# Performance work log

Hardware: AMD Instinct MI355X
Metric: run time of the kernel (lower is better)

The kernel has to match this reference:

```python
import jax, jax.numpy as jnp
import numpy as np

B, N, D, YD = 256, 1024, 64, 2
EPS = 1e-7  # keras SCC epsilon clip


def interleave(x):
    # (B, L, ...): out[:,0::2]=first half, out[:,1::2]=second half
    b, L = x.shape[0], x.shape[1]
    a, c = x[:, : L // 2], x[:, L // 2:]
    return jnp.stack([a, c], axis=2).reshape((b, L) + x.shape[2:])


def block_interleave(x, scope):
    # tf.split into N//scope chunks of size `scope`, Interleave each, concat
    b, L = x.shape[0], x.shape[1]
    rest = x.shape[2:]
    xr = x.reshape((b, L // scope, 2, scope // 2) + rest)
    xr = jnp.swapaxes(xr, 2, 3)
    return xr.reshape((b, L) + rest)


def split_even_odd(x):
    # returns (odd, even) = (x[:,0::2], x[:,1::2])
    return x[:, 0::2], x[:, 1::2]


def mlp2(x, W1, b1, W2, b2):
    return jnp.dot(jax.nn.relu(jnp.dot(x, W1) + b1), W2) + b2


def emb2llr(e, W, b):
    return jax.nn.softmax(jnp.dot(e, W) + b, axis=-1)


def scce(v, p):
    # v: (B,L,1) int labels, p: (B,L,2) probs -> (B,L) per-element NLL
    pt = jnp.take_along_axis(p, v, axis=-1)[..., 0]
    return -jnp.log(jnp.clip(pt, EPS, 1.0))


def setup_inputs() -> dict:
    key = jax.random.key(0)
    ks = jax.random.split(key, 16)
    s = lambda fan: 1.0 / np.sqrt(fan)
    return {
        "x": jax.random.randint(ks[0], (B, N, 1), 0, 2, dtype=jnp.int32),
        "y": jax.random.normal(ks[1], (B, N, YD), dtype=jnp.float32),
        "emb_W": jax.random.normal(ks[2], (YD, D), dtype=jnp.float32) * s(YD),
        "emb_b": jnp.zeros((D,), jnp.float32),
        "lab_emb": jax.random.normal(ks[3], (2, D), dtype=jnp.float32) * s(D),
        "cn_W1": jax.random.normal(ks[4], (2 * D, D), dtype=jnp.float32) * s(2 * D),
        "cn_b1": jnp.zeros((D,), jnp.float32),
        "cn_W2": jax.random.normal(ks[5], (D, D), dtype=jnp.float32) * s(D),
        "cn_b2": jnp.zeros((D,), jnp.float32),
        "bn_W1": jax.random.normal(ks[6], (3 * D, D), dtype=jnp.float32) * s(3 * D),
        "bn_b1": jnp.zeros((D,), jnp.float32),
        "bn_W2": jax.random.normal(ks[7], (D, D), dtype=jnp.float32) * s(D),
        "bn_b2": jnp.zeros((D,), jnp.float32),
        "llr_W": jax.random.normal(ks[8], (D, 2), dtype=jnp.float32) * s(D),
        "llr_b": jnp.zeros((2,), jnp.float32),
    }


def reference(x, y, emb_W, emb_b, lab_emb, cn_W1, cn_b1, cn_W2, cn_b2,
              bn_W1, bn_b1, bn_W2, bn_b2, llr_W, llr_b):
    v = x.astype(jnp.int32)  # (B,N,1)
    e = jnp.dot(y, emb_W) + emb_b  # (B,N,D) observation embedding

    losses, preds, norms = [], [], []
    pred = emb2llr(e, llr_W, llr_b)
    losses.append(scce(v, pred))
    preds.append(pred)
    norms.append(jnp.linalg.norm(e, axis=-1))

    scope = 2
    while scope <= N:
        v_il = block_interleave(v, scope)
        v_odd, v_even = split_even_odd(v_il)
        v_xor = jnp.mod(v_odd + v_even, 2)  # (B,N/2,1)
        v_prime = interleave(jnp.concatenate((v_xor, v_even), axis=1))

        e_il = block_interleave(e, scope)
        e_odd, e_even = split_even_odd(e_il)  # (B,N/2,D) each
        v_xor_emb = lab_emb[v_xor[..., 0]]  # (B,N/2,D)

        e1_left = mlp2(jnp.concatenate((e_odd, e_even), axis=-1),
                       cn_W1, cn_b1, cn_W2, cn_b2)
        e1_right = mlp2(jnp.concatenate((e_odd, e_even, v_xor_emb), axis=-1),
                        bn_W1, bn_b1, bn_W2, bn_b2)
        e_prime = interleave(jnp.concatenate((e1_left, e1_right), axis=1))

        pred = emb2llr(e_prime, llr_W, llr_b)
        losses.append(scce(v_prime, pred))
        preds.append(pred)
        norms.append(jnp.linalg.norm(e_prime, axis=-1))

        v, e = v_prime, e_prime
        scope *= 2

    return (jnp.stack(losses, axis=-2),   # (B, S, N)
            jnp.stack(preds, axis=-2),    # (B, N, S, 2)
            jnp.stack(norms, axis=-2))    # (B, S, N)
```

## Files before the change

### kernel.cpp

```cpp
#include <hip/hip_runtime.h>
#include <hip/hip_bf16.h>

#define NB 256
#define NN 1024
#define NSTAGES 11
#define EPSF 1e-7f

typedef unsigned short u16;
typedef unsigned int u32;
typedef unsigned long long u64;
typedef __attribute__((ext_vector_type(8))) short short8;
typedef __attribute__((ext_vector_type(16))) float f32x16;

static constexpr size_t PRED_BASE = (size_t)NB * NSTAGES * NN;
static constexpr size_t NORM_BASE = PRED_BASE + (size_t)NB * NN * NSTAGES * 2;

static constexpr int LW_OFF = 24576;

__device__ __forceinline__ u16 f2bf(float f) {
  unsigned u = __float_as_uint(f);
  unsigned r = (u + 0x7fffu + ((u >> 16) & 1u)) >> 16;
  return (u16)r;
}
__device__ __forceinline__ unsigned pack_bf2(float a, float b) {
  __hip_bfloat162 h = __float22bfloat162_rn(make_float2(a, b));
  return *(unsigned*)&h;
}
__device__ __forceinline__ u32 spread16(u32 v) {
  v = (v | (v << 8)) & 0x00FF00FFu;
  v = (v | (v << 4)) & 0x0F0F0F0Fu;
  v = (v | (v << 2)) & 0x33333333u;
  v = (v | (v << 1)) & 0x55555555u;
  return v;
}
__device__ __forceinline__ void emit_out(float* __restrict__ out, int b, int n, int s,
                                         float z0, float z1, float nrm2, int label) {
  float m  = fmaxf(z0, z1);
  float p0 = expf(z0 - m), p1 = expf(z1 - m);
  float inv = 1.0f / (p0 + p1);
  p0 *= inv; p1 *= inv;
  float pt = label ? p1 : p0;
  pt = fminf(fmaxf(pt, EPSF), 1.0f);
  out[((size_t)b * NSTAGES + s) * NN + n] = -logf(pt);
  size_t pb = PRED_BASE + (((size_t)b * NN + n) * NSTAGES + s) * 2;
  out[pb + 0] = p0;
  out[pb + 1] = p1;
  out[NORM_BASE + ((size_t)b * NSTAGES + s) * NN + n] = sqrtf(nrm2);
}

__device__ __forceinline__ int eaddr(int row, int c16) {
  return row * 64 + (((c16) ^ (row & 7)) << 3);
}
__device__ __forceinline__ int eaddr32(int row, int m31) {
  return row * 64 + (((((m31) >> 2) ^ (row & 7)) << 3) | (((m31) & 3) << 1));
}

__global__ __launch_bounds__(256) void prep_kernel(
    const float* __restrict__ cn_W1, const float* __restrict__ bn_W1,
    const float* __restrict__ cn_W2, const float* __restrict__ bn_W2,
    const float* __restrict__ lab_emb, const float* __restrict__ llr_W,
    const float* __restrict__ bn_b1,
    u16* __restrict__ wfrag, float* __restrict__ labW_g) {
  int t = blockIdx.x * 256 + threadIdx.x;
  if (t < 3072) {
    int f = t >> 6, l = t & 63, h = l >> 5, c = l & 31;
    const float* src; int ks, nt;
    if (f < 16)      { src = cn_W1; ks = f >> 1; nt = f & 1; }
    else if (f < 32) { int g = f - 16; src = bn_W1; ks = g >> 1; nt = g & 1; }
    else if (f < 40) { int g = f - 32; src = cn_W2; ks = g >> 1; nt = g & 1; }
    else             { int g = f - 40; src = bn_W2; ks = g >> 1; nt = g & 1; }
    int col = 2 * c + nt;
    u16 vals[8];
    #pragma unroll
    for (int j = 0; j < 8; ++j) {
      int k = ks * 16 + h * 8 + j;
      vals[j] = f2bf(src[k * 64 + col]);
    }
    uint4 u;
    u.x = (unsigned)vals[0] | ((unsigned)vals[1] << 16);
    u.y = (unsigned)vals[2] | ((unsigned)vals[3] << 16);
    u.z = (unsigned)vals[4] | ((unsigned)vals[5] << 16);
    u.w = (unsigned)vals[6] | ((unsigned)vals[7] << 16);
    *(uint4*)(wfrag + (size_t)t * 8) = u;
  } else if (t < 3136) {
    int k = t - 3072;
    unsigned wv = (unsigned)f2bf(llr_W[k * 2]) | ((unsigned)f2bf(llr_W[k * 2 + 1]) << 16);
    ((unsigned*)(wfrag + LW_OFF))[k] = wv;
  } else if (t < 3264) {
    int idx = t - 3136;
    int v = idx >> 6, c = idx & 63;
    float acc = bn_b1[c];
    for (int d = 0; d < 64; ++d)
      acc = fmaf(lab_emb[v * 64 + d], bn_W1[(128 + d) * 64 + c], acc);
    labW_g[idx] = acc;
  }
}

#define BFR(FI) (((FI) < 28) ? *(const short8*)(wlds + (FI) * 512 + ln * 8) \
                             : *(const short8*)(wfrag + (FI) * 512 + ln * 8))

__global__ __launch_bounds__(512) void polar_kernel(
    const int* __restrict__ x, const float* __restrict__ y,
    const float* __restrict__ emb_W, const float* __restrict__ emb_b,
    const u16* __restrict__ wfrag, const float* __restrict__ labW_g,
    const float* __restrict__ cn_b1, const float* __restrict__ cn_b2,
    const float* __restrict__ bn_b2, const float* __restrict__ llr_W,
    const float* __restrict__ llr_b, float* __restrict__ out) {
  __shared__ __align__(16) u16 eL[NN * 64];
  __shared__ __align__(16) u16 wlds[28 * 512];
  __shared__ u32 vmask[2][32];
  __shared__ float labW[2][64];

  const int tid = threadIdx.x;
  const int w = tid >> 6, ln = tid & 63;
  const int m31 = ln & 31, h8 = ln >> 5;
  const int b = blockIdx.x;

  for (int i = tid; i < 28 * 64; i += 512)
    ((uint4*)wlds)[i] = ((const uint4*)wfrag)[i];
  if (tid < 128) ((float*)labW)[tid] = labW_g[tid];

  const float lb0 = llr_b[0], lb1 = llr_b[1];
  const float2 cb1 = *(const float2*)(cn_b1 + 2 * m31);
  const float2 cb2 = *(const float2*)(cn_b2 + 2 * m31);
  const float2 bb2 = *(const float2*)(bn_b2 + 2 * m31);

  #pragma unroll
  for (int rep = 0; rep < 2; ++rep) {
    int n = rep * 512 + tid;
    float2 yv = *(const float2*)(y + ((size_t)b * NN + n) * 2);
    float z0 = lb0, z1 = lb1, nr = 0.f;
    #pragma unroll
    for (int o8 = 0; o8 < 8; ++o8) {
      u32 vals[4];
      #pragma unroll
      for (int jj = 0; jj < 4; ++jj) {
        int o = o8 * 8 + jj * 2;
        float e0 = fmaf(yv.x, emb_W[o],     fmaf(yv.y, emb_W[64 + o],     emb_b[o]));
        float e1 = fmaf(yv.x, emb_W[o + 1], fmaf(yv.y, emb_W[64 + o + 1], emb_b[o + 1]));
        vals[jj] = pack_bf2(e0, e1);
        z0 = fmaf(e0, llr_W[o * 2 + 0], z0); z1 = fmaf(e0, llr_W[o * 2 + 1], z1);
        nr = fmaf(e0, e0, nr);
        z0 = fmaf(e1, llr_W[o * 2 + 2], z0); z1 = fmaf(e1, llr_W[o * 2 + 3], z1);
        nr = fmaf(e1, e1, nr);
      }
      uint4 q; q.x = vals[0]; q.y = vals[1]; q.z = vals[2]; q.w = vals[3];
      *(uint4*)(eL + eaddr(n, o8)) = q;
    }
    int v = x[(size_t)b * NN + n] & 1;
    emit_out(out, b, n, 0, z0, z1, nr, v);
    u64 bm = __ballot(v != 0);
    if (ln == 0)  vmask[0][rep * 16 + 2 * w]     = (u32)bm;
    if (ln == 32) vmask[0][rep * 16 + 2 * w + 1] = (u32)(bm >> 32);
  }
  __syncthreads();

  const float2 lwv0 = *(const float2*)(&labW[0][2 * m31]);
  const float2 lwv1 = *(const float2*)(&labW[1][2 * m31]);

  #pragma unroll 1
  for (int s = 1; s <= 10; ++s) {
    const int sh = s - 1;
    const int half = 1 << sh;
    const u32* vmR = vmask[(s - 1) & 1];
    u32* vmW = vmask[s & 1];

    short8 Ao[2][4], Ae[2][4];
    int io[2], ie[2], vo[2], ve[2], vx[2];
    u32 bxs[2];
    #pragma unroll
    for (int t = 0; t < 2; ++t) {
      int i = 64 * w + 32 * t + m31;
      int g = i >> sh, u = i & (half - 1);
      io[t] = g * (half << 1) + u;
      ie[t] = io[t] + half;
      #pragma unroll
      for (int f = 0; f < 4; ++f) {
        Ao[t][f] = *(const short8*)(eL + eaddr(io[t], f * 2 + h8));
        Ae[t][f] = *(const short8*)(eL + eaddr(ie[t], f * 2 + h8));
      }
      vo[t] = (vmR[io[t] >> 5] >> (io[t] & 31)) & 1;
      ve[t] = (vmR[ie[t] >> 5] >> (ie[t] & 31)) & 1;
      vx[t] = vo[t] ^ ve[t];
      u32 bx = (u32)__ballot(vx[t] != 0);
      u32 be = (u32)__ballot(ve[t] != 0);
      bxs[t] = bx;
      u32 lo = spread16(bx & 0xffffu) | (spread16(be & 0xffffu) << 1);
      u32 hi = spread16(bx >> 16) | (spread16(be >> 16) << 1);
      if (ln == 0) { vmW[4 * w + 2 * t] = lo; vmW[4 * w + 2 * t + 1] = hi; }
    }
    __syncthreads();

    if (s >= 2) {
      const uint4* lwq = (const uint4*)(wfrag + LW_OFF);
      uint4 lq[4][2];
      #pragma unroll
      for (int f = 0; f < 4; ++f) {
        lq[f][0] = lwq[f * 4 + h8 * 2];
        lq[f][1] = lwq[f * 4 + h8 * 2 + 1];
      }
      #pragma unroll
      for (int t = 0; t < 2; ++t) {
        #pragma unroll
        for (int side = 0; side < 2; ++side) {
          float z0 = 0.f, z1 = 0.f, nr = 0.f;
          #pragma unroll
          for (int f = 0; f < 4; ++f) {
            short8 av8 = side ? Ae[t][f] : Ao[t][f];
            #pragma unroll
            for (int j = 0; j < 8; ++j) {
              u32 pv = ((const u32*)&av8)[j >> 1];
              float val = __uint_as_float((j & 1) ? (pv & 0xffff0000u) : (pv << 16));
              u32 lwp = (j < 4) ? ((const u32*)&lq[f][0])[j] : ((const u32*)&lq[f][1])[j - 4];
              z0 = fmaf(val, __uint_as_float(lwp << 16), z0);
              z1 = fmaf(val, __uint_as_float(lwp & 0xffff0000u), z1);
              nr = fmaf(val, val, nr);
            }
          }
          z0 += __shfl_xor(z0, 32);
          z1 += __shfl_xor(z1, 32);
          nr += __shfl_xor(nr, 32);
          if (h8 == 0)
            emit_out(out, b, side ? ie[t] : io[t], s - 1,
                     z0 + lb0, z1 + lb1, nr, side ? ve[t] : vo[t]);
        }
      }
    }

    f32x16 a0[2], a1[2];
    #pragma unroll
    for (int t = 0; t < 2; ++t)
      #pragma unroll
      for (int r = 0; r < 16; ++r) { a0[t][r] = cb1.x; a1[t][r] = cb1.y; }
    #pragma unroll
    for (int ks = 0; ks < 8; ++ks) {
      short8 B0 = BFR(ks * 2 + 0);
      short8 B1 = BFR(ks * 2 + 1);
      #pragma unroll
      for (int t = 0; t < 2; ++t) {
        short8 a = (ks < 4) ? Ao[t][ks] : Ae[t][ks - 4];
        a0[t] = __builtin_amdgcn_mfma_f32_32x32x16_bf16(a, B0, a0[t], 0, 0, 0);
        a1[t] = __builtin_amdgcn_mfma_f32_32x32x16_bf16(a, B1, a1[t], 0, 0, 0);
      }
    }
    #pragma unroll
    for (int t = 0; t < 2; ++t) {
      int obase = 128 * w + 64 * t;
      #pragma unroll
      for (int r = 0; r < 16; ++r) {
        int row = (r & 3) + 8 * (r >> 2) + 4 * h8;
        int R = obase + 2 * row;
        *(u32*)(eL + eaddr32(R, m31)) =
            pack_bf2(fmaxf(a0[t][r], 0.f), fmaxf(a1[t][r], 0.f));
      }
    }

    #pragma unroll
    for (int t = 0; t < 2; ++t)
      #pragma unroll
      for (int r = 0; r < 16; ++r) {
        int row = (r & 3) + 8 * (r >> 2) + 4 * h8;
        int bit = (bxs[t] >> row) & 1;
        a0[t][r] = bit ? lwv1.x : lwv0.x;
        a1[t][r] = bit ? lwv1.y : lwv0.y;
      }
    #pragma unroll
    for (int ks = 0; ks < 8; ++ks) {
      short8 B0 = BFR(16 + ks * 2 + 0);
      short8 B1 = BFR(16 + ks * 2 + 1);
      #pragma unroll
      for (int t = 0; t < 2; ++t) {
        short8 a = (ks < 4) ? Ao[t][ks] : Ae[t][ks - 4];
        a0[t] = __builtin_amdgcn_mfma_f32_32x32x16_bf16(a, B0, a0[t], 0, 0, 0);
        a1[t] = __builtin_amdgcn_mfma_f32_32x32x16_bf16(a, B1, a1[t], 0, 0, 0);
      }
    }
    #pragma unroll
    for (int t = 0; t < 2; ++t) {
      int obase = 128 * w + 64 * t;
      #pragma unroll
      for (int r = 0; r < 16; ++r) {
        int row = (r & 3) + 8 * (r >> 2) + 4 * h8;
        int R = obase + 2 * row + 1;
        *(u32*)(eL + eaddr32(R, m31)) =
            pack_bf2(fmaxf(a0[t][r], 0.f), fmaxf(a1[t][r], 0.f));
      }
    }

    {
      short8 Hc[2][4];
      #pragma unroll
      for (int t = 0; t < 2; ++t) {
        int R = 128 * w + 64 * t + 2 * m31;
        #pragma unroll
        for (int f = 0; f < 4; ++f)
          Hc[t][f] = *(const short8*)(eL + eaddr(R, f * 2 + h8));
      }
      f32x16 d0[2], d1[2];
      #pragma unroll
      for (int t = 0; t < 2; ++t)
        #pragma unroll
        for (int r = 0; r < 16; ++r) { d0[t][r] = cb2.x; d1[t][r] = cb2.y; }
      #pragma unroll
      for (int ks = 0; ks < 4; ++ks) {
        short8 B0 = BFR(32 + ks * 2 + 0);
        short8 B1 = BFR(32 + ks * 2 + 1);
        #pragma unroll
        for (int t = 0; t < 2; ++t) {
          d0[t] = __builtin_amdgcn_mfma_f32_32x32x16_bf16(Hc[t][ks], B0, d0[t], 0, 0, 0);
          d1[t] = __builtin_amdgcn_mfma_f32_32x32x16_bf16(Hc[t][ks], B1, d1[t], 0, 0, 0);
        }
      }
      #pragma unroll
      for (int t = 0; t < 2; ++t) {
        int obase = 128 * w + 64 * t;
        #pragma unroll
        for (int r = 0; r < 16; ++r) {
          int row = (r & 3) + 8 * (r >> 2) + 4 * h8;
          int R = obase + 2 * row;
          *(u32*)(eL + eaddr32(R, m31)) = pack_bf2(d0[t][r], d1[t][r]);
        }
      }
    }

    {
      short8 Hb[2][4];
      #pragma unroll
      for (int t = 0; t < 2; ++t) {
        int R = 128 * w + 64 * t + 2 * m31 + 1;
        #pragma unroll
        for (int f = 0; f < 4; ++f)
          Hb[t][f] = *(const short8*)(eL + eaddr(R, f * 2 + h8));
      }
      f32x16 d0[2], d1[2];
      #pragma unroll
      for (int t = 0; t < 2; ++t)
        #pragma unroll
        for (int r = 0; r < 16; ++r) { d0[t][r] = bb2.x; d1[t][r] = bb2.y; }
      #pragma unroll
      for (int ks = 0; ks < 4; ++ks) {
        short8 B0 = BFR(40 + ks * 2 + 0);
        short8 B1 = BFR(40 + ks * 2 + 1);
        #pragma unroll
        for (int t = 0; t < 2; ++t) {
          d0[t] = __builtin_amdgcn_mfma_f32_32x32x16_bf16(Hb[t][ks], B0, d0[t], 0, 0, 0);
          d1[t] = __builtin_amdgcn_mfma_f32_32x32x16_bf16(Hb[t][ks], B1, d1[t], 0, 0, 0);
        }
      }
      #pragma unroll
      for (int t = 0; t < 2; ++t) {
        int obase = 128 * w + 64 * t;
        #pragma unroll
        for (int r = 0; r < 16; ++r) {
          int row = (r & 3) + 8 * (r >> 2) + 4 * h8;
          int R = obase + 2 * row + 1;
          *(u32*)(eL + eaddr32(R, m31)) = pack_bf2(d0[t][r], d1[t][r]);
        }
      }
    }
    __syncthreads();
  }

  {
    const uint4* lwq = (const uint4*)(wfrag + LW_OFF);
    uint4 lq[4][2];
    #pragma unroll
    for (int f = 0; f < 4; ++f) {
      lq[f][0] = lwq[f * 4 + h8 * 2];
      lq[f][1] = lwq[f * 4 + h8 * 2 + 1];
    }
    #pragma unroll
    for (int it = 0; it < 4; ++it) {
      int n = 128 * w + 32 * it + m31;
      float z0 = 0.f, z1 = 0.f, nr = 0.f;
      #pragma unroll
      for (int f = 0; f < 4; ++f) {
        short8 av8 = *(const short8*)(eL + eaddr(n, f * 2 + h8));
        #pragma unroll
        for (int j = 0; j < 8; ++j) {
          u32 pv = ((const u32*)&av8)[j >> 1];
          float val = __uint_as_float((j & 1) ? (pv & 0xffff0000u) : (pv << 16));
          u32 lwp = (j < 4) ? ((const u32*)&lq[f][0])[j] : ((const u32*)&lq[f][1])[j - 4];
          z0 = fmaf(val, __uint_as_float(lwp << 16), z0);
          z1 = fmaf(val, __uint_as_float(lwp & 0xffff0000u), z1);
          nr = fmaf(val, val, nr);
        }
      }
      z0 += __shfl_xor(z0, 32);
      z1 += __shfl_xor(z1, 32);
      nr += __shfl_xor(nr, 32);
      int lab = (vmask[0][n >> 5] >> (n & 31)) & 1;
      if (h8 == 0) emit_out(out, b, n, NSTAGES - 1, z0 + lb0, z1 + lb1, nr, lab);
    }
  }
}

extern "C" void kernel_launch(void* const* d_in, const int* in_sizes, int n_in,
                              void* d_out, int out_size, void* d_ws, size_t ws_size,
                              hipStream_t stream) {
  const int*   x      = (const int*)d_in[0];
  const float* y      = (const float*)d_in[1];
  const float* emb_W  = (const float*)d_in[2];
  const float* emb_b  = (const float*)d_in[3];
  const float* labemb = (const float*)d_in[4];
  const float* cn_W1  = (const float*)d_in[5];
  const float* cn_b1  = (const float*)d_in[6];
  const float* cn_W2  = (const float*)d_in[7];
  const float* cn_b2  = (const float*)d_in[8];
  const float* bn_W1  = (const float*)d_in[9];
  const float* bn_b1  = (const float*)d_in[10];
  const float* bn_W2  = (const float*)d_in[11];
  const float* bn_b2  = (const float*)d_in[12];
  const float* llr_W  = (const float*)d_in[13];
  const float* llr_b  = (const float*)d_in[14];
  float* out = (float*)d_out;

  u16* wfrag = (u16*)d_ws;
  float* labW_g = (float*)((char*)d_ws + 65536);

  prep_kernel<<<13, 256, 0, stream>>>(cn_W1, bn_W1, cn_W2, bn_W2, labemb, llr_W,
                                      bn_b1, wfrag, labW_g);
  polar_kernel<<<NB, 512, 0, stream>>>(x, y, emb_W, emb_b, wfrag, labW_g,
                                       cn_b1, cn_b2, bn_b2, llr_W, llr_b, out);
}
```

Before: 281.7 us.

## Stage per-stage probabilities in LDS and write preds contiguously at end

Each stage now writes its softmax probabilities into a shared-memory staging buffer. At the next stage every thread pulls its two entries into registers. At the end, each thread writes all 11 stages' (p0,p1) pairs for its positions as contiguous float2 stores, replacing strided scattered global stores. The weight fragments cached in LDS drop from 28 to 23 to make room for the staging buffer, so more weight loads go to global memory. The change also adds 44 registers per thread for the accumulated predictions, which may raise register pressure.

```diff
diff --git a/kernel.cpp b/kernel.cpp
--- a/kernel.cpp
+++ b/kernel.cpp
@@ -16,6 +16,8 @@
 static constexpr size_t NORM_BASE = PRED_BASE + (size_t)NB * NN * NSTAGES * 2;
 
 static constexpr int LW_OFF = 24576;
+
+#define WLDS_FR 23
 
 __device__ __forceinline__ u16 f2bf(float f) {
   unsigned u = __float_as_uint(f);
@@ -33,7 +35,8 @@
   v = (v | (v << 1)) & 0x55555555u;
   return v;
 }
-__device__ __forceinline__ void emit_out(float* __restrict__ out, int b, int n, int s,
+__device__ __forceinline__ void emit_out(float* __restrict__ out, float* __restrict__ pstage,
+                                         int b, int n, int s,
                                          float z0, float z1, float nrm2, int label) {
   float m  = fmaxf(z0, z1);
   float p0 = expf(z0 - m), p1 = expf(z1 - m);
@@ -42,9 +45,7 @@
   float pt = label ? p1 : p0;
   pt = fminf(fmaxf(pt, EPSF), 1.0f);
   out[((size_t)b * NSTAGES + s) * NN + n] = -logf(pt);
-  size_t pb = PRED_BASE + (((size_t)b * NN + n) * NSTAGES + s) * 2;
-  out[pb + 0] = p0;
-  out[pb + 1] = p1;
+  *(float2*)(pstage + 2 * n) = make_float2(p0, p1);
   out[NORM_BASE + ((size_t)b * NSTAGES + s) * NN + n] = sqrtf(nrm2);
 }
 
@@ -96,8 +97,8 @@
   }
 }
 
-#define BFR(FI) (((FI) < 28) ? *(const short8*)(wlds + (FI) * 512 + ln * 8) \
-                             : *(const short8*)(wfrag + (FI) * 512 + ln * 8))
+#define BFR(FI) (((FI) < WLDS_FR) ? *(const short8*)(wlds + (FI) * 512 + ln * 8) \
+                                  : *(const short8*)(wfrag + (FI) * 512 + ln * 8))
 
 __global__ __launch_bounds__(512) void polar_kernel(
     const int* __restrict__ x, const float* __restrict__ y,
@@ -107,16 +108,19 @@
     const float* __restrict__ bn_b2, const float* __restrict__ llr_W,
     const float* __restrict__ llr_b, float* __restrict__ out) {
   __shared__ __align__(16) u16 eL[NN * 64];
-  __shared__ __align__(16) u16 wlds[28 * 512];
+  __shared__ __align__(16) u16 wlds[WLDS_FR * 512];
   __shared__ u32 vmask[2][32];
   __shared__ float labW[2][64];
+  __shared__ __align__(8) float pstage[NN * 2];
 
   const int tid = threadIdx.x;
   const int w = tid >> 6, ln = tid & 63;
   const int m31 = ln & 31, h8 = ln >> 5;
   const int b = blockIdx.x;
 
-  for (int i = tid; i < 28 * 64; i += 512)
+  float2 accP[2][NSTAGES];
+
+  for (int i = tid; i < WLDS_FR * 64; i += 512)
     ((uint4*)wlds)[i] = ((const uint4*)wfrag)[i];
   if (tid < 128) ((float*)labW)[tid] = labW_g[tid];
 
@@ -148,7 +152,7 @@
       *(uint4*)(eL + eaddr(n, o8)) = q;
     }
     int v = x[(size_t)b * NN + n] & 1;
-    emit_out(out, b, n, 0, z0, z1, nr, v);
+    emit_out(out, pstage, b, n, 0, z0, z1, nr, v);
     u64 bm = __ballot(v != 0);
     if (ln == 0)  vmask[0][rep * 16 + 2 * w]     = (u32)bm;
     if (ln == 32) vmask[0][rep * 16 + 2 * w + 1] = (u32)(bm >> 32);
@@ -160,6 +164,22 @@
 
   #pragma unroll 1
   for (int s = 1; s <= 10; ++s) {
+    if (s >= 2) {
+      float2 pv0 = *(const float2*)(pstage + 2 * tid);
+      float2 pv1 = *(const float2*)(pstage + 2 * (512 + tid));
+      switch (s) {
+        case 2:  accP[0][0] = pv0; accP[1][0] = pv1; break;
+        case 3:  accP[0][1] = pv0; accP[1][1] = pv1; break;
+        case 4:  accP[0][2] = pv0; accP[1][2] = pv1; break;
+        case 5:  accP[0][3] = pv0; accP[1][3] = pv1; break;
+        case 6:  accP[0][4] = pv0; accP[1][4] = pv1; break;
+        case 7:  accP[0][5] = pv0; accP[1][5] = pv1; break;
+        case 8:  accP[0][6] = pv0; accP[1][6] = pv1; break;
+        case 9:  accP[0][7] = pv0; accP[1][7] = pv1; break;
+        default: accP[0][8] = pv0; accP[1][8] = pv1; break;
+      }
+    }
+
     const int sh = s - 1;
     const int half = 1 << sh;
     const u32* vmR = vmask[(s - 1) & 1];
@@ -221,7 +241,7 @@
           z1 += __shfl_xor(z1, 32);
           nr += __shfl_xor(nr, 32);
           if (h8 == 0)
-            emit_out(out, b, side ? ie[t] : io[t], s - 1,
+            emit_out(out, pstage, b, side ? ie[t] : io[t], s - 1,
                      z0 + lb0, z1 + lb1, nr, side ? ve[t] : vo[t]);
         }
       }
@@ -359,6 +379,12 @@
       }
     }
     __syncthreads();
+  }
+
+  {
+    float2 pv0 = *(const float2*)(pstage + 2 * tid);
+    float2 pv1 = *(const float2*)(pstage + 2 * (512 + tid));
+    accP[0][9] = pv0; accP[1][9] = pv1;
   }
 
   {
@@ -390,8 +416,23 @@
       z1 += __shfl_xor(z1, 32);
       nr += __shfl_xor(nr, 32);
       int lab = (vmask[0][n >> 5] >> (n & 31)) & 1;
-      if (h8 == 0) emit_out(out, b, n, NSTAGES - 1, z0 + lb0, z1 + lb1, nr, lab);
-    }
+      if (h8 == 0) emit_out(out, pstage, b, n, NSTAGES - 1, z0 + lb0, z1 + lb1, nr, lab);
+    }
+  }
+  __syncthreads();
+  {
+    float2 pv0 = *(const float2*)(pstage + 2 * tid);
+    float2 pv1 = *(const float2*)(pstage + 2 * (512 + tid));
+    accP[0][10] = pv0; accP[1][10] = pv1;
+  }
+
+  #pragma unroll
+  for (int rep = 0; rep < 2; ++rep) {
+    int n = rep * 512 + tid;
+    float* dst = out + PRED_BASE + ((size_t)b * NN + n) * (NSTAGES * 2);
+    #pragma unroll
+    for (int sj = 0; sj < NSTAGES; ++sj)
+      *(float2*)(dst + 2 * sj) = accP[rep][sj];
   }
 }
 
```

New measurement: 302.2 us. +7.3%, slower.
